# Kernel optimization log

Measured on AMD Instinct MI355X. Metric: run time of the kernel, lower is better.

Reference implementation:

```python
import jax, jax.numpy as jnp
import numpy as np

CODEBOOK_DIM = 64
CODEBOOK_SLOTS = 512
TEMPERATURE = 0.5
BS, H, W = 16, 64, 64
EPS_G = 1e-10  # gumbel numerical floor
EPS_P = 1e-9   # matches probs.add(1e-09) in torch code


def setup_inputs() -> dict:
    key = jax.random.key(0)
    k1, k2, k3 = jax.random.split(key, 3)
    ze = jax.random.normal(k1, (BS, CODEBOOK_DIM, H, W), dtype=jnp.float32)
    codebook = jax.random.normal(k2, (CODEBOOK_SLOTS, CODEBOOK_DIM), dtype=jnp.float32)
    # uniform noise for Gumbel reparameterization of RelaxedOneHotCategorical.rsample
    u = jax.random.uniform(k3, (BS * H * W, CODEBOOK_SLOTS), dtype=jnp.float32)
    return {"ze": ze, "codebook": codebook, "u": u}


def reference(ze, codebook, u):
    bs, d, h, w = ze.shape
    K = codebook.shape[0]
    log_K = jnp.log(jnp.float32(K))
    # [bs, d, h, w] -> [N, d]
    ze_flat = jnp.transpose(ze, (0, 2, 3, 1)).reshape(-1, d)
    # squared euclidean distances via addmm: ||c||^2 + ||z||^2 - 2 z c^T  -> [N, K]
    distances = (
        jnp.sum(codebook * codebook, axis=1)[None, :]
        + jnp.sum(ze_flat * ze_flat, axis=1, keepdims=True)
        - 2.0 * (ze_flat @ codebook.T)
    )
    logits = -distances
    # Gumbel-softmax (relaxed one-hot categorical rsample)
    gumbel = -jnp.log(-jnp.log(u + EPS_G) + EPS_G)
    soft_onehot = jax.nn.softmax((logits + gumbel) / TEMPERATURE, axis=1)
    hard_indices = jnp.argmax(soft_onehot, axis=1).reshape(bs, h, w)
    # weighted codebook lookup: [N, K] @ [K, d] -> [bs, h, w, d] -> [bs, d, h, w]
    z_q = jnp.transpose((soft_onehot @ codebook).reshape(bs, h, w, d), (0, 3, 1, 2))
    probs = jax.nn.softmax(logits, axis=1)
    KL = jnp.mean(jnp.sum((probs * (jnp.log(probs + EPS_P) + log_K)).reshape(bs, -1), axis=1))
    commit_loss = jnp.mean(jnp.sum((probs * distances).reshape(bs, -1), axis=1))
    return (z_q, hard_indices, KL, commit_loss)
```

## Files before the change

### kernel.cpp

```cpp
#include <hip/hip_runtime.h>
#include <math.h>
#include <stdint.h>

#define IDX_OFF 4194304
#define KL_OFF  4259840
#define CM_OFF  4259841
#define LOG_K   6.238324625039508f
#define THR     2.0f

typedef _Float16 half8 __attribute__((ext_vector_type(8)));
typedef _Float16 half4 __attribute__((ext_vector_type(4)));
typedef float    f32x4 __attribute__((ext_vector_type(4)));

__global__ __launch_bounds__(64) void vq_pack(const float* __restrict__ cbk, void* __restrict__ ws){
  _Float16* LAh = (_Float16*)ws;
  _Float16* LAl = LAh + 32768;
  _Float16* QAh = LAl + 32768;
  float*    CCw = (float*)(QAh + 32768);
  const int slot = blockIdx.x, c = threadIdx.x;
  const float x = cbk[(slot << 6) + c];
  const _Float16 h = (_Float16)x;
  const _Float16 l = (_Float16)(x - (float)h);
  const int g = slot >> 4;
  {
    const int kc = c >> 5, quad = (c >> 3) & 3, j = c & 7;
    const int lane = (quad << 4) | (slot & 15);
    const int idx = ((((g << 1) | kc) << 6) | lane) * 8 + j;
    LAh[idx] = h; LAl[idx] = l;
  }
  {
    const int quad2 = (slot >> 2) & 3, j2 = slot & 3;
    const int cg = c >> 4;
    const int lane = (quad2 << 4) | (c & 15);
    QAh[(((g << 6) | lane) << 4) | (cg << 2) | j2] = h;
  }
  float s = x * x;
#pragma unroll
  for (int m = 1; m < 64; m <<= 1) s += __shfl_xor(s, m, 64);
  if (c == 0) CCw[slot] = s;
}

__global__ __launch_bounds__(256, 4) void vq_main(
    const float* __restrict__ ze, const float* __restrict__ uin,
    const void* __restrict__ ws, float* __restrict__ out)
{
  __shared__ float RED[8];
  const _Float16* wsp = (const _Float16*)ws;
  const half8* LAh = (const half8*)wsp;
  const half8* LAl = (const half8*)(wsp + 32768);
  const half4* QAh = (const half4*)(wsp + 65536);
  const float* CCw = (const float*)(wsp + 98304);

  const int tid  = threadIdx.x;
  const int lane = tid & 63, l15 = lane & 15, quad = lane >> 4;
  const int wv   = tid >> 6;
  const int n    = (blockIdx.x << 6) | (wv << 4) | l15;
  const int bb   = n >> 12, hh = (n >> 6) & 63, w = n & 63;

  const float* zp = ze + ((size_t)bb << 18) + (hh << 6) + w;
  half8 zh[2], zl[2];
  float zz = 0.f;
#pragma unroll
  for (int kc = 0; kc < 2; ++kc)
#pragma unroll
    for (int j = 0; j < 8; ++j){
      const float x = zp[(size_t)((kc << 5) + (quad << 3) + j) << 12];
      zz = fmaf(x, x, zz);
      const _Float16 h = (_Float16)x;
      zh[kc][j] = h;
      zl[kc][j] = (_Float16)(x - (float)h);
    }
  zz += __shfl_xor(zz, 16, 64);
  zz += __shfl_xor(zz, 32, 64);

  float m1 = -3.0e38f, s1 = 0.f, s2s = 0.f, t1s = 0.f, am = -3.0e38f;
  int   ki = 0;
  f32x4 zq0 = {0.f,0.f,0.f,0.f}, zq1 = {0.f,0.f,0.f,0.f};
  f32x4 zq2 = {0.f,0.f,0.f,0.f}, zq3 = {0.f,0.f,0.f,0.f};

  const float* uB = uin + ((size_t)n << 9) + (quad << 2);

#pragma unroll 2
  for (int g = 0; g < 32; ++g){
    const float4 uf = *(const float4*)(uB + (g << 4));
    const float4 c4 = *(const float4*)(CCw + (g << 4) + (quad << 2));
    const half8 ch0 = LAh[((g << 1) | 0) * 64 + lane];
    const half8 ch1 = LAh[((g << 1) | 1) * 64 + lane];
    const half8 cl0 = LAl[((g << 1) | 0) * 64 + lane];
    const half8 cl1 = LAl[((g << 1) | 1) * 64 + lane];
    const int qb = ((g << 6) | lane) << 2;
    const half4 qa0 = QAh[qb | 0], qa1 = QAh[qb | 1];
    const half4 qa2 = QAh[qb | 2], qa3 = QAh[qb | 3];

    f32x4 acc = {0.f,0.f,0.f,0.f};
    acc = __builtin_amdgcn_mfma_f32_16x16x32_f16(ch0, zh[0], acc, 0,0,0);
    acc = __builtin_amdgcn_mfma_f32_16x16x32_f16(cl0, zh[0], acc, 0,0,0);
    acc = __builtin_amdgcn_mfma_f32_16x16x32_f16(ch0, zl[0], acc, 0,0,0);
    acc = __builtin_amdgcn_mfma_f32_16x16x32_f16(ch1, zh[1], acc, 0,0,0);
    acc = __builtin_amdgcn_mfma_f32_16x16x32_f16(cl1, zh[1], acc, 0,0,0);
    acc = __builtin_amdgcn_mfma_f32_16x16x32_f16(ch1, zl[1], acc, 0,0,0);

    const float ua[4] = {uf.x, uf.y, uf.z, uf.w};
    const float ca[4] = {c4.x, c4.y, c4.z, c4.w};
    float lg[4], lu[4], av[4];
#pragma unroll
    for (int r = 0; r < 4; ++r){
      lg[r] = fmaf(2.f, acc[r], -ca[r] - zz);
      lu[r] = 1e-10f - __logf(ua[r] + 1e-10f);
      av[r] = lg[r] - __logf(lu[r]);
    }
    float pm = fmaxf(fmaxf(av[0], av[1]), fmaxf(av[2], av[3]));
    pm = fmaxf(pm, __shfl_xor(pm, 16, 64));
    pm = fmaxf(pm, __shfl_xor(pm, 32, 64));
    if (pm > m1 + THR){
      const float sc = __expf(m1 - pm), sc2 = sc * sc;
      s1 *= sc2; s2s *= sc; t1s *= sc;
      zq0 *= sc2; zq1 *= sc2; zq2 *= sc2; zq3 *= sc2;
      m1 = pm;
    }
    half4 ef;
    const int sb = (g << 4) | (quad << 2);
#pragma unroll
    for (int r = 0; r < 4; ++r){
      const float t = __expf(av[r] - m1);
      const float e = t * t;
      s1 += e;
      ef[r] = (_Float16)e;
      const float p = t * lu[r];
      s2s += p;
      t1s = fmaf(p, lg[r], t1s);
      if (av[r] > am){ am = av[r]; ki = sb + r; }
    }
    zq0 = __builtin_amdgcn_mfma_f32_16x16x16f16(qa0, ef, zq0, 0,0,0);
    zq1 = __builtin_amdgcn_mfma_f32_16x16x16f16(qa1, ef, zq1, 0,0,0);
    zq2 = __builtin_amdgcn_mfma_f32_16x16x16f16(qa2, ef, zq2, 0,0,0);
    zq3 = __builtin_amdgcn_mfma_f32_16x16x16f16(qa3, ef, zq3, 0,0,0);
  }

#pragma unroll
  for (int m = 16; m < 64; m <<= 1){
    s1  += __shfl_xor(s1,  m, 64);
    s2s += __shfl_xor(s2s, m, 64);
    t1s += __shfl_xor(t1s, m, 64);
    const float vo = __shfl_xor(am, m, 64);
    const int   io = __shfl_xor(ki, m, 64);
    if (vo > am || (vo == am && io < ki)){ am = vo; ki = io; }
  }
  const float inv = 1.0f / s1;
  const float pl  = t1s / s2s;
  float kl = pl + LOG_K - m1 - __logf(s2s);
  float cm = -pl;
  if (quad == 0) out[IDX_OFF + n] = (float)ki;

  float* ob = out + ((size_t)bb << 18) + (hh << 6) + w;
#pragma unroll
  for (int r = 0; r < 4; ++r){
    const int cb = (quad << 2) + r;
    ob[(size_t)(cb     ) << 12] = zq0[r] * inv;
    ob[(size_t)(cb + 16) << 12] = zq1[r] * inv;
    ob[(size_t)(cb + 32) << 12] = zq2[r] * inv;
    ob[(size_t)(cb + 48) << 12] = zq3[r] * inv;
  }

  if (quad != 0){ kl = 0.f; cm = 0.f; }
#pragma unroll
  for (int m = 1; m < 16; m <<= 1){ kl += __shfl_xor(kl, m, 64); cm += __shfl_xor(cm, m, 64); }
#pragma unroll
  for (int m = 16; m < 64; m <<= 1){ kl += __shfl_xor(kl, m, 64); cm += __shfl_xor(cm, m, 64); }
  if (lane == 0){ RED[wv] = kl; RED[wv + 4] = cm; }
  __syncthreads();
  if (tid == 0){
    atomicAdd(out + KL_OFF, (RED[0]+RED[1]+RED[2]+RED[3]) * 0.0625f);
    atomicAdd(out + CM_OFF, (RED[4]+RED[5]+RED[6]+RED[7]) * 0.0625f);
  }
}

extern "C" void kernel_launch(void* const* d_in, const int* in_sizes, int n_in,
                              void* d_out, int out_size, void* d_ws, size_t ws_size,
                              hipStream_t stream){
  const float* ze  = (const float*)d_in[0];
  const float* cbk = (const float*)d_in[1];
  const float* uin = (const float*)d_in[2];
  float* out = (float*)d_out;
  hipMemsetAsync(out + KL_OFF, 0, 2 * sizeof(float), stream);
  vq_pack<<<dim3(512), dim3(64), 0, stream>>>(cbk, d_ws);
  vq_main<<<dim3(1024), dim3(256), 0, stream>>>(ze, uin, d_ws, out);
}
```

Baseline: 261.0 us.

## Split codebook slots across two wave halves and merge softmax state via LDS

Doubles the block to 512 threads so each group of 16 points is handled by two waves, each sweeping half of the 512 codebook slots. After the loop, the second half writes its partial online-softmax state (max, sums, z_q accumulators, argmax) to shared memory, and the first half merges it with rescaling before writing outputs. The goal is more waves in flight to hide the latency of the u loads and the MFMA chain, at the cost of an extra LDS exchange, a barrier, and duplicated ze loads and conversions per wave. QA loads are also widened from four half4 reads to two half8 reads.

```diff
diff --git a/kernel.cpp b/kernel.cpp
--- a/kernel.cpp
+++ b/kernel.cpp
@@ -40,21 +40,22 @@
   if (c == 0) CCw[slot] = s;
 }
 
-__global__ __launch_bounds__(256, 4) void vq_main(
+__global__ __launch_bounds__(512, 8) void vq_main(
     const float* __restrict__ ze, const float* __restrict__ uin,
     const void* __restrict__ ws, float* __restrict__ out)
 {
+  __shared__ float LX[4*22*64];
   __shared__ float RED[8];
   const _Float16* wsp = (const _Float16*)ws;
   const half8* LAh = (const half8*)wsp;
   const half8* LAl = (const half8*)(wsp + 32768);
-  const half4* QAh = (const half4*)(wsp + 65536);
+  const half8* QA8 = (const half8*)(wsp + 65536);
   const float* CCw = (const float*)(wsp + 98304);
 
   const int tid  = threadIdx.x;
   const int lane = tid & 63, l15 = lane & 15, quad = lane >> 4;
-  const int wv   = tid >> 6;
-  const int n    = (blockIdx.x << 6) | (wv << 4) | l15;
+  const int wv   = tid >> 6, pg = wv & 3, half = wv >> 2;
+  const int n    = (blockIdx.x << 6) | (pg << 4) | l15;
   const int bb   = n >> 12, hh = (n >> 6) & 63, w = n & 63;
 
   const float* zp = ze + ((size_t)bb << 18) + (hh << 6) + w;
@@ -78,19 +79,20 @@
   f32x4 zq0 = {0.f,0.f,0.f,0.f}, zq1 = {0.f,0.f,0.f,0.f};
   f32x4 zq2 = {0.f,0.f,0.f,0.f}, zq3 = {0.f,0.f,0.f,0.f};
 
-  const float* uB = uin + ((size_t)n << 9) + (quad << 2);
+  const float* uB = uin + ((size_t)n << 9) + (half << 8) + (quad << 2);
+  const int gbase = half << 4;
 
 #pragma unroll 2
-  for (int g = 0; g < 32; ++g){
+  for (int g = 0; g < 16; ++g){
+    const int gl = gbase + g;
     const float4 uf = *(const float4*)(uB + (g << 4));
-    const float4 c4 = *(const float4*)(CCw + (g << 4) + (quad << 2));
-    const half8 ch0 = LAh[((g << 1) | 0) * 64 + lane];
-    const half8 ch1 = LAh[((g << 1) | 1) * 64 + lane];
-    const half8 cl0 = LAl[((g << 1) | 0) * 64 + lane];
-    const half8 cl1 = LAl[((g << 1) | 1) * 64 + lane];
-    const int qb = ((g << 6) | lane) << 2;
-    const half4 qa0 = QAh[qb | 0], qa1 = QAh[qb | 1];
-    const half4 qa2 = QAh[qb | 2], qa3 = QAh[qb | 3];
+    const float4 c4 = *(const float4*)(CCw + (gl << 4) + (quad << 2));
+    const half8 ch0 = LAh[((gl << 1) | 0) * 64 + lane];
+    const half8 ch1 = LAh[((gl << 1) | 1) * 64 + lane];
+    const half8 cl0 = LAl[((gl << 1) | 0) * 64 + lane];
+    const half8 cl1 = LAl[((gl << 1) | 1) * 64 + lane];
+    const half8 qa01 = QA8[((gl << 6) | lane) * 2 + 0];
+    const half8 qa23 = QA8[((gl << 6) | lane) * 2 + 1];
 
     f32x4 acc = {0.f,0.f,0.f,0.f};
     acc = __builtin_amdgcn_mfma_f32_16x16x32_f16(ch0, zh[0], acc, 0,0,0);
@@ -119,7 +121,7 @@
       m1 = pm;
     }
     half4 ef;
-    const int sb = (g << 4) | (quad << 2);
+    const int sb = (gl << 4) | (quad << 2);
 #pragma unroll
     for (int r = 0; r < 4; ++r){
       const float t = __expf(av[r] - m1);
@@ -131,6 +133,10 @@
       t1s = fmaf(p, lg[r], t1s);
       if (av[r] > am){ am = av[r]; ki = sb + r; }
     }
+    const half4 qa0 = __builtin_shufflevector(qa01, qa01, 0,1,2,3);
+    const half4 qa1 = __builtin_shufflevector(qa01, qa01, 4,5,6,7);
+    const half4 qa2 = __builtin_shufflevector(qa23, qa23, 0,1,2,3);
+    const half4 qa3 = __builtin_shufflevector(qa23, qa23, 4,5,6,7);
     zq0 = __builtin_amdgcn_mfma_f32_16x16x16f16(qa0, ef, zq0, 0,0,0);
     zq1 = __builtin_amdgcn_mfma_f32_16x16x16f16(qa1, ef, zq1, 0,0,0);
     zq2 = __builtin_amdgcn_mfma_f32_16x16x16f16(qa2, ef, zq2, 0,0,0);
@@ -146,28 +152,61 @@
     const int   io = __shfl_xor(ki, m, 64);
     if (vo > am || (vo == am && io < ki)){ am = vo; ki = io; }
   }
-  const float inv = 1.0f / s1;
-  const float pl  = t1s / s2s;
-  float kl = pl + LOG_K - m1 - __logf(s2s);
-  float cm = -pl;
-  if (quad == 0) out[IDX_OFF + n] = (float)ki;
-
-  float* ob = out + ((size_t)bb << 18) + (hh << 6) + w;
-#pragma unroll
-  for (int r = 0; r < 4; ++r){
-    const int cb = (quad << 2) + r;
-    ob[(size_t)(cb     ) << 12] = zq0[r] * inv;
-    ob[(size_t)(cb + 16) << 12] = zq1[r] * inv;
-    ob[(size_t)(cb + 32) << 12] = zq2[r] * inv;
-    ob[(size_t)(cb + 48) << 12] = zq3[r] * inv;
-  }
-
-  if (quad != 0){ kl = 0.f; cm = 0.f; }
-#pragma unroll
-  for (int m = 1; m < 16; m <<= 1){ kl += __shfl_xor(kl, m, 64); cm += __shfl_xor(cm, m, 64); }
-#pragma unroll
-  for (int m = 16; m < 64; m <<= 1){ kl += __shfl_xor(kl, m, 64); cm += __shfl_xor(cm, m, 64); }
-  if (lane == 0){ RED[wv] = kl; RED[wv + 4] = cm; }
+
+  float* X = &LX[(pg * 22) * 64 + lane];
+  if (half == 1){
+#pragma unroll
+    for (int r = 0; r < 4; ++r){
+      X[(r     ) << 6] = zq0[r];
+      X[(r +  4) << 6] = zq1[r];
+      X[(r +  8) << 6] = zq2[r];
+      X[(r + 12) << 6] = zq3[r];
+    }
+    X[16 << 6] = s1;  X[17 << 6] = s2s; X[18 << 6] = t1s;
+    X[19 << 6] = m1;  X[20 << 6] = am;  X[21 << 6] = __int_as_float(ki);
+  }
+  __syncthreads();
+  if (half == 0){
+    const float m1B = X[19 << 6];
+    const float M   = fmaxf(m1, m1B);
+    const float sA  = __expf(m1 - M),  sB  = __expf(m1B - M);
+    const float sA2 = sA * sA,         sB2 = sB * sB;
+    s1  = s1  * sA2 + X[16 << 6] * sB2;
+    s2s = s2s * sA  + X[17 << 6] * sB;
+    t1s = t1s * sA  + X[18 << 6] * sB;
+    const float amB = X[20 << 6];
+    const int   kiB = __float_as_int(X[21 << 6]);
+    if (amB > am || (amB == am && kiB < ki)){ am = amB; ki = kiB; }
+    m1 = M;
+#pragma unroll
+    for (int r = 0; r < 4; ++r){
+      zq0[r] = zq0[r] * sA2 + X[(r     ) << 6] * sB2;
+      zq1[r] = zq1[r] * sA2 + X[(r +  4) << 6] * sB2;
+      zq2[r] = zq2[r] * sA2 + X[(r +  8) << 6] * sB2;
+      zq3[r] = zq3[r] * sA2 + X[(r + 12) << 6] * sB2;
+    }
+
+    const float inv = 1.0f / s1;
+    const float pl  = t1s / s2s;
+    float kl = pl + LOG_K - m1 - __logf(s2s);
+    float cm = -pl;
+    if (quad == 0) out[IDX_OFF + n] = (float)ki;
+
+    float* ob = out + ((size_t)bb << 18) + (hh << 6) + w;
+#pragma unroll
+    for (int r = 0; r < 4; ++r){
+      const int cb = (quad << 2) + r;
+      ob[(size_t)(cb     ) << 12] = zq0[r] * inv;
+      ob[(size_t)(cb + 16) << 12] = zq1[r] * inv;
+      ob[(size_t)(cb + 32) << 12] = zq2[r] * inv;
+      ob[(size_t)(cb + 48) << 12] = zq3[r] * inv;
+    }
+
+    if (quad != 0){ kl = 0.f; cm = 0.f; }
+#pragma unroll
+    for (int m = 1; m < 64; m <<= 1){ kl += __shfl_xor(kl, m, 64); cm += __shfl_xor(cm, m, 64); }
+    if (lane == 0){ RED[pg] = kl; RED[pg + 4] = cm; }
+  }
   __syncthreads();
   if (tid == 0){
     atomicAdd(out + KL_OFF, (RED[0]+RED[1]+RED[2]+RED[3]) * 0.0625f);
@@ -184,5 +223,5 @@
   float* out = (float*)d_out;
   hipMemsetAsync(out + KL_OFF, 0, 2 * sizeof(float), stream);
   vq_pack<<<dim3(512), dim3(64), 0, stream>>>(cbk, d_ws);
-  vq_main<<<dim3(1024), dim3(256), 0, stream>>>(ze, uin, d_ws, out);
+  vq_main<<<dim3(1024), dim3(512), 0, stream>>>(ze, uin, d_ws, out);
 }
```

Result: slower. 476.7 us (+82.6%).
